# Optimization experiments

Measured on AMD Instinct MI355X. Metric: run time of the kernel, lower is better.

## Reference

```python
import jax, jax.numpy as jnp
import numpy as np

ALPHA = 1.0
BETA = 10.0
OHEM_RATIO = 3
DB_K = 50.0
EPS_P = 1e-7  # clamp probs so log() stays finite (torch BCELoss clamps log at -100)

N, H, W = 16, 640, 640


def setup_inputs() -> dict:
    key = jax.random.key(0)
    k1, k2, k3, k4 = jax.random.split(key, 4)
    return {
        "outputs": jax.random.uniform(k1, (N, 2, H, W), dtype=jnp.float32),
        "labels": jax.random.uniform(k2, (N, 2, H, W), dtype=jnp.float32),
        "training_masks": jax.random.uniform(k3, (N, H, W), dtype=jnp.float32),
        "G_d": jax.random.uniform(k4, (N, H, W), dtype=jnp.float32),
    }


def _ohem_single(score, gt, tm):
    # score, gt, tm: [H, W] for one sample
    pos = (gt > 0.5) & (tm > 0.5)
    neg = (gt <= 0.5) & (tm > 0.5)
    pos_num = pos.sum()
    neg_avail = neg.sum()
    neg_num = jnp.minimum(pos_num * OHEM_RATIO, neg_avail)
    # descending sort of negative-pixel scores; non-neg pixels pushed to -inf
    flat = jnp.where(neg, score, -jnp.inf).ravel()
    sorted_desc = jnp.sort(flat)[::-1]
    idx = jnp.clip(neg_num - 1, 0, flat.shape[0] - 1)
    thr = sorted_desc[idx]
    sel = ((score >= thr) & neg) | pos
    sel = jnp.where(neg_num == 0, pos, sel)          # no negatives selectable -> pos only
    sel = jnp.where(pos_num == 0, tm > 0.5, sel)     # no positives -> whole training mask
    return sel


def _masked_bce(p, t, m):
    # masked-mean BCE == gathering masked elems then BCELoss(mean)
    t = (t > 0.5).astype(p.dtype)
    p = jnp.clip(p, EPS_P, 1.0 - EPS_P)
    loss = -(t * jnp.log(p) + (1.0 - t) * jnp.log1p(-p))
    msum = m.sum()
    return jnp.where(msum > 0, (loss * m).sum() / msum, jnp.zeros((), p.dtype))


def reference(outputs, labels, training_masks, G_d):
    prob_map = outputs[:, 0, :, :]
    thres_map = outputs[:, 1, :, :]
    gt_prob = labels[:, 0, :, :]
    gt_thres = labels[:, 1, :, :]

    sel = jax.vmap(_ohem_single)(prob_map, gt_prob, training_masks)
    sel = sel.astype(prob_map.dtype)  # boolean-derived: no gradient path

    loss_prob = _masked_bce(prob_map, gt_prob, sel)
    bin_map = jax.nn.sigmoid(DB_K * (prob_map - thres_map))  # differentiable binarization
    loss_bin = _masked_bce(bin_map, gt_prob, sel)
    loss_thres = (jnp.abs(thres_map - gt_thres) * G_d).sum() / (G_d.sum() + 1e-6)

    loss_all = loss_prob + ALPHA * loss_bin + BETA * loss_thres
    return (loss_all, loss_prob, loss_bin, loss_thres)
```

## Files before the change

### kernel.cpp

```cpp
#include <hip/hip_runtime.h>
#include <math.h>
#include <stdint.h>

#define NS    16
#define HWSZ  409600
#define NF4   102400
#define NBIN  128
#define SLW   (NBIN + 8)
#define CAP   4096
#define BCAP  512
#define SBPS  100
#define GBPS  100
#define PADI  32

typedef unsigned long long u64;
typedef float f32x4 __attribute__((ext_vector_type(4)));

__device__ __forceinline__ unsigned fkey(float f) {
    unsigned u = __float_as_uint(f);
    if (u == 0x80000000u) u = 0u;
    return (u & 0x80000000u) ? ~u : (u | 0x80000000u);
}

__device__ __forceinline__ void bce_pair(float pv, float tv, bool tc, float& o1, float& o2) {
    float pc = fminf(fmaxf(pv, 1e-7f), 1.0f - 1e-7f);
    float a = tc ? pc : 1.0f - pc;
    o1 = -__logf(a);
    float x = 50.0f * (pv - tv);
    float y = tc ? -x : x;
    float t2 = __expf(-fabsf(y));
    float sp = __logf(1.0f + t2);
    sp = (y > 0.0f) ? y + sp : sp;
    o2 = fminf(sp, 16.118095651f);
}

__device__ __forceinline__ int pbin(float p) {
    int b = (int)(p * (float)NBIN);
    return min(max(b, 0), NBIN - 1);
}

__device__ __forceinline__ bool wave_find(const int* __restrict__ h, int nbins, int k,
                                          int* bin_out, int* rank_out) {
    const int lane = threadIdx.x & 63;
    const int CH = nbins >> 6;
    const int topStart = nbins - 1 - lane * CH;
    int s = 0;
    for (int b = 0; b < CH; ++b) s += h[topStart - b];
    int incl = s;
    for (int off = 1; off < 64; off <<= 1) {
        int v = __shfl_up(incl, off, 64);
        if (lane >= off) incl += v;
    }
    int before = incl - s;
    if (before < k && k <= incl) {
        int c = before;
        for (int b = 0; b < CH; ++b) {
            int hb = h[topStart - b];
            c += hb;
            if (c >= k) { *bin_out = topStart - b; *rank_out = k - (c - hb); return true; }
        }
    }
    return false;
}

#define GLOAD(dst, addr) \
    asm volatile("global_load_dwordx4 %0, %1, off" : "=v"(dst) : "v"(addr))
#define LOADSET(Sp, St, Sg, Sq, Sm, Sd, idx) do { \
    GLOAD(Sp, P + (idx));  GLOAD(St, Th + (idx)); GLOAD(Sg, G + (idx)); \
    GLOAD(Sq, Gt + (idx)); GLOAD(Sm, T + (idx)); GLOAD(Sd, D + (idx)); } while (0)
#define WAITSET(Sp, St, Sg, Sq, Sm, Sd, N) \
    asm volatile("s_waitcnt vmcnt(" #N ")" \
                 : "+v"(Sp), "+v"(St), "+v"(Sg), "+v"(Sq), "+v"(Sm), "+v"(Sd))

__global__ void k_scan1(const float* __restrict__ outputs, const float* __restrict__ labels,
                        const float* __restrict__ tmask, const float* __restrict__ gd,
                        float* __restrict__ part) {
    __shared__ int lc[NBIN];
    __shared__ float rf[4][6];
    __shared__ int ri[4][2];
    const int t = threadIdx.x, n = blockIdx.y, lane = t & 63, wid = t >> 6;
    if (t < NBIN) lc[t] = 0;
    __syncthreads();
    const f32x4* P  = (const f32x4*)(outputs + (size_t)n * 2 * HWSZ);
    const f32x4* Th = P + NF4;
    const f32x4* G  = (const f32x4*)(labels + (size_t)n * 2 * HWSZ);
    const f32x4* Gt = G + NF4;
    const f32x4* T  = (const f32x4*)(tmask + (size_t)n * HWSZ);
    const f32x4* D  = (const f32x4*)(gd + (size_t)n * HWSZ);
    const int i0 = blockIdx.x * 1024 + t;
    float s3 = 0.f, s4 = 0.f, p1 = 0.f, p2 = 0.f, n1 = 0.f, n2 = 0.f;
    int cp = 0, cn = 0;
    auto proc = [&](const f32x4& p, const f32x4& th, const f32x4& g, const f32x4& q,
                    const f32x4& m, const f32x4& d) {
#pragma unroll
        for (int e = 0; e < 4; ++e) {
            float pv = p[e], tv = th[e], gv = g[e], qv = q[e], mv = m[e], dv = d[e];
            s3 += fabsf(tv - qv) * dv;
            s4 += dv;
            bool msk = mv > 0.5f, tc = gv > 0.5f;
            if (msk) {
                float o1, o2; bce_pair(pv, tv, tc, o1, o2);
                if (tc) { p1 += o1; p2 += o2; cp++; }
                else    { n1 += o1; n2 += o2; cn++; atomicAdd(&lc[pbin(pv)], 1); }
            }
        }
    };
    f32x4 ap, at, ag, aq, am, ad, bp, bt, bg, bq, bm, bd, cq, ct, cg, cqq, cm, cd;
    LOADSET(ap, at, ag, aq, am, ad, i0);
    LOADSET(bp, bt, bg, bq, bm, bd, i0 + 256);
    LOADSET(cq, ct, cg, cqq, cm, cd, i0 + 512);
    WAITSET(ap, at, ag, aq, am, ad, 12);
    proc(ap, at, ag, aq, am, ad);
    LOADSET(ap, at, ag, aq, am, ad, i0 + 768);
    WAITSET(bp, bt, bg, bq, bm, bd, 12);
    proc(bp, bt, bg, bq, bm, bd);
    WAITSET(cq, ct, cg, cqq, cm, cd, 6);
    proc(cq, ct, cg, cqq, cm, cd);
    WAITSET(ap, at, ag, aq, am, ad, 0);
    proc(ap, at, ag, aq, am, ad);
    for (int off = 32; off; off >>= 1) {
        p1 += __shfl_down(p1, off, 64);
        p2 += __shfl_down(p2, off, 64);
        n1 += __shfl_down(n1, off, 64);
        n2 += __shfl_down(n2, off, 64);
        s3 += __shfl_down(s3, off, 64);
        s4 += __shfl_down(s4, off, 64);
        cp += __shfl_down(cp, off, 64);
        cn += __shfl_down(cn, off, 64);
    }
    if (!lane) {
        rf[wid][0] = p1; rf[wid][1] = p2; rf[wid][2] = n1;
        rf[wid][3] = n2; rf[wid][4] = s3; rf[wid][5] = s4;
        ri[wid][0] = cp; ri[wid][1] = cn;
    }
    __syncthreads();
    float* slice = part + (size_t)(n * SBPS + blockIdx.x) * SLW;
    int* slice_i = (int*)slice;
    if (t < NBIN) slice_i[t] = lc[t];
    if (!t) {
        slice_i[NBIN + 0] = ri[0][0] + ri[1][0] + ri[2][0] + ri[3][0];
        slice_i[NBIN + 1] = ri[0][1] + ri[1][1] + ri[2][1] + ri[3][1];
#pragma unroll
        for (int i = 0; i < 6; ++i)
            slice[NBIN + 2 + i] = rf[0][i] + rf[1][i] + rf[2][i] + rf[3][i];
    }
}

__global__ void k_sel1(const float* __restrict__ part,
                       int* __restrict__ mode, int* __restrict__ b1o, int* __restrict__ k1o,
                       int* __restrict__ poss,
                       double* __restrict__ psum, double* __restrict__ abD, int* __restrict__ abc,
                       double* __restrict__ s3s, double* __restrict__ s4s,
                       int* __restrict__ cand_cnt, unsigned* __restrict__ done) {
    __shared__ int lc[NBIN];
    __shared__ double sdr[4][6];
    __shared__ int sir[4][2];
    __shared__ int ric[4];
    __shared__ int sb1, sk1, s_md, s_k;
    const int n = blockIdx.x, t = threadIdx.x, lane = t & 63, wid = t >> 6;
    if (t < PADI) cand_cnt[n * PADI + t] = 0;
    if (!n && !t) *done = 0u;
    const float* base = part + (size_t)n * SBPS * SLW;
    double v[6] = {0, 0, 0, 0, 0, 0};
    int cp = 0, cn = 0;
    if (t < SBPS) {
        const float* sl = base + (size_t)t * SLW;
        const int* sli = (const int*)sl;
        cp = sli[NBIN + 0]; cn = sli[NBIN + 1];
#pragma unroll
        for (int i = 0; i < 6; ++i) v[i] = (double)sl[NBIN + 2 + i];
    }
    for (int off = 32; off; off >>= 1) {
#pragma unroll
        for (int i = 0; i < 6; ++i) v[i] += __shfl_down(v[i], off, 64);
        cp += __shfl_down(cp, off, 64);
        cn += __shfl_down(cn, off, 64);
    }
    if (!lane) {
#pragma unroll
        for (int i = 0; i < 6; ++i) sdr[wid][i] = v[i];
        sir[wid][0] = cp; sir[wid][1] = cn;
    }
    __syncthreads();
    if (!t) {
        int pos = sir[0][0] + sir[1][0] + sir[2][0] + sir[3][0];
        int neg = sir[0][1] + sir[1][1] + sir[2][1] + sir[3][1];
        double c[6];
#pragma unroll
        for (int i = 0; i < 6; ++i) c[i] = sdr[0][i] + sdr[1][i] + sdr[2][i] + sdr[3][i];
        int k = pos * 3; if (k > neg) k = neg;
        int md = (pos == 0) ? 2 : ((k == 0) ? 1 : ((k == neg) ? 3 : 0));
        mode[n] = md;
        poss[n] = pos;
        psum[n * 2 + 0] = c[0];
        psum[n * 2 + 1] = c[1];
        s3s[n] = c[4];
        s4s[n] = c[5];
        if (md == 1)      { abD[n * 16] = 0.0;  abD[n * 16 + 1] = 0.0;  abc[n] = 0; }
        else if (md != 0) { abD[n * 16] = c[2]; abD[n * 16 + 1] = c[3]; abc[n] = neg; }
        else              { abD[n * 16] = 0.0;  abD[n * 16 + 1] = 0.0; }
        s_md = md; s_k = k;
    }
    __syncthreads();
    if (s_md != 0) return;
    if (t < NBIN) lc[t] = 0;
    __syncthreads();
    {
        const int bin = t & (NBIN - 1);
        const int j0 = (t < NBIN) ? 0 : SBPS / 2;
        const int j1 = (t < NBIN) ? SBPS / 2 : SBPS;
        int c = 0;
        for (int j = j0; j < j1; ++j) c += ((const int*)(base + (size_t)j * SLW))[bin];
        atomicAdd(&lc[bin], c);
    }
    __syncthreads();
    if (t < 64) { int b, r; if (wave_find(lc, NBIN, s_k, &b, &r)) { sb1 = b; sk1 = r; } }
    __syncthreads();
    const int B = sb1;
    if (!t) { b1o[n] = sb1; k1o[n] = sk1; }
    int ac = (t < NBIN && t > B) ? lc[t] : 0;
    for (int off = 32; off; off >>= 1) ac += __shfl_down(ac, off, 64);
    if (!lane) ric[wid] = ac;
    __syncthreads();
    if (!t) abc[n] = ric[0] + ric[1] + ric[2] + ric[3];
}

__global__ void k_gather(const float* __restrict__ outputs, const float* __restrict__ labels,
                         const float* __restrict__ tmask,
                         const int* __restrict__ mode, const int* __restrict__ b1a,
                         int* __restrict__ cand_cnt, unsigned* __restrict__ ck,
                         float* __restrict__ cv1, float* __restrict__ cv2,
                         double* __restrict__ abD) {
    const int n = blockIdx.y;
    if (mode[n] != 0) return;
    const int b1n = b1a[n];
    __shared__ int lcnt, lbase;
    __shared__ unsigned lsk[BCAP];
    __shared__ float lv1[BCAP], lv2[BCAP];
    __shared__ double rdd[4][2];
    const int t = threadIdx.x, lane = t & 63, wid = t >> 6;
    if (!t) lcnt = 0;
    __syncthreads();
    const float* bp = outputs + (size_t)n * 2 * HWSZ;
    const float4* P  = (const float4*)bp;
    const float4* Th = P + NF4;
    const float4* G  = (const float4*)(labels + (size_t)n * 2 * HWSZ);
    const float4* T  = (const float4*)(tmask + (size_t)n * HWSZ);
    const int stride = GBPS * 256;
    float a1 = 0.f, a2 = 0.f;
    for (int i4 = blockIdx.x * 256 + t; i4 < NF4; i4 += stride) {
        float4 p = P[i4], th = Th[i4], g = G[i4], m = T[i4];
        const float* pp = (const float*)&p;  const float* tt = (const float*)&th;
        const float* gg = (const float*)&g;  const float* mm = (const float*)&m;
#pragma unroll
        for (int e = 0; e < 4; ++e) {
            bool neg = (gg[e] <= 0.5f) && (mm[e] > 0.5f);
            int bin = pbin(pp[e]);
            if (neg && bin >= b1n) {
                float o1, o2; bce_pair(pp[e], tt[e], false, o1, o2);
                if (bin > b1n) { a1 += o1; a2 += o2; }
                else {
                    int idx = atomicAdd(&lcnt, 1);
                    if (idx < BCAP) { lsk[idx] = fkey(pp[e]); lv1[idx] = o1; lv2[idx] = o2; }
                    else {
                        int gi = atomicAdd(&cand_cnt[n * PADI], 1);
                        if (gi < CAP) { ck[n * CAP + gi] = fkey(pp[e]); cv1[n * CAP + gi] = o1; cv2[n * CAP + gi] = o2; }
                    }
                }
            }
        }
    }
    double v0 = a1, v1 = a2;
    for (int off = 32; off; off >>= 1) {
        v0 += __shfl_down(v0, off, 64);
        v1 += __shfl_down(v1, off, 64);
    }
    if (!lane) { rdd[wid][0] = v0; rdd[wid][1] = v1; }
    __syncthreads();
    if (!t) {
        double sA = rdd[0][0] + rdd[1][0] + rdd[2][0] + rdd[3][0];
        double sB = rdd[0][1] + rdd[1][1] + rdd[2][1] + rdd[3][1];
        if (sA != 0.0) atomicAdd(&abD[n * 16], sA);
        if (sB != 0.0) atomicAdd(&abD[n * 16 + 1], sB);
    }
    __syncthreads();
    const int cnt = min(lcnt, BCAP);
    if (!t && cnt) lbase = atomicAdd(&cand_cnt[n * PADI], cnt);
    __syncthreads();
    if (cnt) {
        const int bb = lbase;
        for (int i = t; i < cnt; i += 256) {
            int gi = bb + i;
            if (gi < CAP) { ck[n * CAP + gi] = lsk[i]; cv1[n * CAP + gi] = lv1[i]; cv2[n * CAP + gi] = lv2[i]; }
        }
    }
}

__global__ void k_final(const float* __restrict__ outputs, const float* __restrict__ labels,
                        const float* __restrict__ tmask,
                        const int* __restrict__ mode, const int* __restrict__ b1a,
                        const int* __restrict__ k1a, const int* __restrict__ poss,
                        const int* __restrict__ cand_cnt, const unsigned* __restrict__ ck,
                        const float* __restrict__ cv1, const float* __restrict__ cv2,
                        const double* __restrict__ psum, const double* __restrict__ abD,
                        const int* __restrict__ abc, double* __restrict__ res,
                        const double* __restrict__ s3s, const double* __restrict__ s4s,
                        unsigned* __restrict__ done, float* __restrict__ out) {
    __shared__ unsigned sk[CAP];
    __shared__ float sv1[CAP], sv2[CAP];
    __shared__ int h[2048];
    __shared__ int sbh, srh, sbm, srm, sbl;
    __shared__ double rd[4][2];
    __shared__ int ri[4];
    const int n = blockIdx.x, t = threadIdx.x;
    const int md = mode[n];
    double f1r = 0.0, f2r = 0.0; int fcr = 0;
    if (md == 0) {
        const int k1 = k1a[n];
        const int cc = cand_cnt[n * PADI];
        float f1 = 0.f, f2 = 0.f; int fc = 0;
        if (cc <= CAP) {
            for (int i = t; i < cc; i += 256) {
                sk[i] = ck[n * CAP + i]; sv1[i] = cv1[n * CAP + i]; sv2[i] = cv2[n * CAP + i];
            }
            for (int i = t; i < 2048; i += 256) h[i] = 0;
            __syncthreads();
            for (int i = t; i < cc; i += 256) atomicAdd(&h[sk[i] >> 21], 1);
            __syncthreads();
            if (t < 64) { int b, r; if (wave_find(h, 2048, k1, &b, &r)) { sbh = b; srh = r; } }
            __syncthreads();
            const unsigned bh = (unsigned)sbh; const int r2 = srh;
            for (int i = t; i < 2048; i += 256) h[i] = 0;
            __syncthreads();
            for (int i = t; i < cc; i += 256)
                if ((sk[i] >> 21) == bh) atomicAdd(&h[(sk[i] >> 10) & 0x7FFu], 1);
            __syncthreads();
            if (t < 64) { int b, r; if (wave_find(h, 2048, r2, &b, &r)) { sbm = b; srm = r; } }
            __syncthreads();
            const unsigned bm = (unsigned)sbm; const int r3 = srm;
            for (int i = t; i < 1024; i += 256) h[i] = 0;
            __syncthreads();
            for (int i = t; i < cc; i += 256)
                if ((sk[i] >> 10) == ((bh << 11) | bm)) atomicAdd(&h[sk[i] & 0x3FFu], 1);
            __syncthreads();
            if (t < 64) { int b, r; if (wave_find(h, 1024, r3, &b, &r)) sbl = b; }
            __syncthreads();
            const unsigned thr_key = (bh << 21) | (bm << 10) | (unsigned)sbl;
            for (int i = t; i < cc; i += 256)
                if (sk[i] >= thr_key) { f1 += sv1[i]; f2 += sv2[i]; fc++; }
        } else {
            const int b1n = b1a[n];
            const float* Pp = outputs + (size_t)n * 2 * HWSZ;
            const float* Thp = Pp + HWSZ;
            const float* Gp = labels + (size_t)n * 2 * HWSZ;
            const float* Tp = tmask + (size_t)n * HWSZ;
            for (int i = t; i < 2048; i += 256) h[i] = 0;
            __syncthreads();
            for (int i = t; i < HWSZ; i += 256) {
                float pv = Pp[i];
                if (Gp[i] <= 0.5f && Tp[i] > 0.5f && pbin(pv) == b1n)
                    atomicAdd(&h[fkey(pv) >> 21], 1);
            }
            __syncthreads();
            if (t < 64) { int b, r; if (wave_find(h, 2048, k1, &b, &r)) { sbh = b; srh = r; } }
            __syncthreads();
            const unsigned bh = (unsigned)sbh; const int r2 = srh;
            for (int i = t; i < 2048; i += 256) h[i] = 0;
            __syncthreads();
            for (int i = t; i < HWSZ; i += 256) {
                float pv = Pp[i]; unsigned key = fkey(pv);
                if (Gp[i] <= 0.5f && Tp[i] > 0.5f && pbin(pv) == b1n && (key >> 21) == bh)
                    atomicAdd(&h[(key >> 10) & 0x7FFu], 1);
            }
            __syncthreads();
            if (t < 64) { int b, r; if (wave_find(h, 2048, r2, &b, &r)) { sbm = b; srm = r; } }
            __syncthreads();
            const unsigned bm = (unsigned)sbm; const int r3 = srm;
            for (int i = t; i < 1024; i += 256) h[i] = 0;
            __syncthreads();
            for (int i = t; i < HWSZ; i += 256) {
                float pv = Pp[i]; unsigned key = fkey(pv);
                if (Gp[i] <= 0.5f && Tp[i] > 0.5f && pbin(pv) == b1n && (key >> 10) == ((bh << 11) | bm))
                    atomicAdd(&h[key & 0x3FFu], 1);
            }
            __syncthreads();
            if (t < 64) { int b, r; if (wave_find(h, 1024, r3, &b, &r)) sbl = b; }
            __syncthreads();
            const unsigned thr_key = (bh << 21) | (bm << 10) | (unsigned)sbl;
            for (int i = t; i < HWSZ; i += 256) {
                float pv = Pp[i];
                if (Gp[i] <= 0.5f && Tp[i] > 0.5f && pbin(pv) == b1n && fkey(pv) >= thr_key) {
                    float b1v, b2v; bce_pair(pv, Thp[i], false, b1v, b2v);
                    f1 += b1v; f2 += b2v; fc++;
                }
            }
        }
        double v0 = f1, v1 = f2;
        for (int off = 32; off; off >>= 1) {
            v0 += __shfl_down(v0, off, 64);
            v1 += __shfl_down(v1, off, 64);
            fc += __shfl_down(fc, off, 64);
        }
        const int lane = t & 63, wid = t >> 6;
        if (!lane) { rd[wid][0] = v0; rd[wid][1] = v1; ri[wid] = fc; }
        __syncthreads();
        if (!t) {
            f1r = rd[0][0] + rd[1][0] + rd[2][0] + rd[3][0];
            f2r = rd[0][1] + rd[1][1] + rd[2][1] + rd[3][1];
            fcr = ri[0] + ri[1] + ri[2] + ri[3];
        }
    }
    if (!t) {
        res[n * 3 + 0] = psum[n * 2 + 0] + abD[n * 16] + f1r;
        res[n * 3 + 1] = psum[n * 2 + 1] + abD[n * 16 + 1] + f2r;
        res[n * 3 + 2] = (double)poss[n] + (double)abc[n] + (double)fcr;
        __threadfence();
        unsigned v = atomicAdd(done, 1u);
        if (v == NS - 1) {
            __threadfence();
            double A = 0.0, Bb = 0.0, C = 0.0, S3 = 0.0, S4 = 0.0;
            for (int m = 0; m < NS; ++m) {
                A += res[m * 3 + 0]; Bb += res[m * 3 + 1]; C += res[m * 3 + 2];
                S3 += s3s[m]; S4 += s4s[m];
            }
            double lp = (C > 0.0) ? A / C : 0.0;
            double lb = (C > 0.0) ? Bb / C : 0.0;
            double lt = S3 / (S4 + 1e-6);
            out[0] = (float)(lp + lb + 10.0 * lt);
            out[1] = (float)lp;
            out[2] = (float)lb;
            out[3] = (float)lt;
        }
    }
}

extern "C" void kernel_launch(void* const* d_in, const int* in_sizes, int n_in,
                              void* d_out, int out_size, void* d_ws, size_t ws_size,
                              hipStream_t stream) {
    const float* outputs = (const float*)d_in[0];
    const float* labels  = (const float*)d_in[1];
    const float* tmask   = (const float*)d_in[2];
    const float* gd      = (const float*)d_in[3];
    float* out = (float*)d_out;

    char* ws = (char*)d_ws;
    double* s3s   = (double*)ws;
    double* s4s   = s3s + NS;
    double* psum  = s4s + NS;
    double* abD   = psum + NS * 2;
    double* res   = abD + NS * 16;
    int* abc      = (int*)(res + NS * 3);
    int* mode     = abc + NS;
    int* b1       = mode + NS;
    int* k1       = b1 + NS;
    int* poss     = k1 + NS;
    unsigned* done = (unsigned*)(poss + NS);
    int* cand_cnt = (int*)(done + 8);
    float* part   = (float*)(cand_cnt + NS * PADI);
    unsigned* ck  = (unsigned*)(part + (size_t)NS * SBPS * SLW);
    float* cv1    = (float*)(ck + NS * CAP);
    float* cv2    = cv1 + NS * CAP;
    (void)cv2; (void)ws_size; (void)in_sizes; (void)n_in; (void)out_size;

    k_scan1<<<dim3(SBPS, NS), 256, 0, stream>>>(outputs, labels, tmask, gd, part);
    k_sel1<<<NS, 256, 0, stream>>>(part, mode, b1, k1, poss, psum, abD, abc, s3s, s4s,
                                   cand_cnt, done);
    k_gather<<<dim3(GBPS, NS), 256, 0, stream>>>(outputs, labels, tmask, mode, b1,
                                                 cand_cnt, ck, cv1, cv2, abD);
    k_final<<<NS, 256, 0, stream>>>(outputs, labels, tmask, mode, b1, k1, poss, cand_cnt,
                                    ck, cv1, cv2, psum, abD, abc, res, s3s, s4s, done, out);
}
```

Measured before the change: 39.03 us.

## Fuse gather and final kernels via last-block counter; enlarge scan1 per-block work

Merges the candidate-gather and final-selection kernels into one launch. A per-sample atomic completion counter picks the last gather block, which then runs the radix-select and final reduction, reading candidates straight from global memory instead of staging them in shared memory. This removes one kernel launch and the gap between launches, but the final work now runs serially in a single block per sample after its gather finishes. Scan1 also cuts its blocks per sample from 100 to 80, with each block handling five load sets instead of four, so there are fewer partial slices to reduce at the cost of lower parallelism.

```diff
diff --git a/kernel.cpp b/kernel.cpp
--- a/kernel.cpp
+++ b/kernel.cpp
@@ -9,7 +9,7 @@
 #define SLW   (NBIN + 8)
 #define CAP   4096
 #define BCAP  512
-#define SBPS  100
+#define SBPS  80
 #define GBPS  100
 #define PADI  32
 
@@ -87,7 +87,7 @@
     const f32x4* Gt = G + NF4;
     const f32x4* T  = (const f32x4*)(tmask + (size_t)n * HWSZ);
     const f32x4* D  = (const f32x4*)(gd + (size_t)n * HWSZ);
-    const int i0 = blockIdx.x * 1024 + t;
+    const int i0 = blockIdx.x * 1280 + t;
     float s3 = 0.f, s4 = 0.f, p1 = 0.f, p2 = 0.f, n1 = 0.f, n2 = 0.f;
     int cp = 0, cn = 0;
     auto proc = [&](const f32x4& p, const f32x4& th, const f32x4& g, const f32x4& q,
@@ -114,10 +114,13 @@
     LOADSET(ap, at, ag, aq, am, ad, i0 + 768);
     WAITSET(bp, bt, bg, bq, bm, bd, 12);
     proc(bp, bt, bg, bq, bm, bd);
-    WAITSET(cq, ct, cg, cqq, cm, cd, 6);
+    LOADSET(bp, bt, bg, bq, bm, bd, i0 + 1024);
+    WAITSET(cq, ct, cg, cqq, cm, cd, 12);
     proc(cq, ct, cg, cqq, cm, cd);
-    WAITSET(ap, at, ag, aq, am, ad, 0);
+    WAITSET(ap, at, ag, aq, am, ad, 6);
     proc(ap, at, ag, aq, am, ad);
+    WAITSET(bp, bt, bg, bq, bm, bd, 0);
+    proc(bp, bt, bg, bq, bm, bd);
     for (int off = 32; off; off >>= 1) {
         p1 += __shfl_down(p1, off, 64);
         p2 += __shfl_down(p2, off, 64);
@@ -151,7 +154,8 @@
                        int* __restrict__ poss,
                        double* __restrict__ psum, double* __restrict__ abD, int* __restrict__ abc,
                        double* __restrict__ s3s, double* __restrict__ s4s,
-                       int* __restrict__ cand_cnt, unsigned* __restrict__ done) {
+                       int* __restrict__ cand_cnt, unsigned* __restrict__ gdone,
+                       unsigned* __restrict__ fdone) {
     __shared__ int lc[NBIN];
     __shared__ double sdr[4][6];
     __shared__ int sir[4][2];
@@ -159,7 +163,7 @@
     __shared__ int sb1, sk1, s_md, s_k;
     const int n = blockIdx.x, t = threadIdx.x, lane = t & 63, wid = t >> 6;
     if (t < PADI) cand_cnt[n * PADI + t] = 0;
-    if (!n && !t) *done = 0u;
+    if (!t) { gdone[n] = 0u; if (!n) *fdone = 0u; }
     const float* base = part + (size_t)n * SBPS * SLW;
     double v[6] = {0, 0, 0, 0, 0, 0};
     int cp = 0, cn = 0;
@@ -225,107 +229,103 @@
     if (!t) abc[n] = ric[0] + ric[1] + ric[2] + ric[3];
 }
 
-__global__ void k_gather(const float* __restrict__ outputs, const float* __restrict__ labels,
-                         const float* __restrict__ tmask,
-                         const int* __restrict__ mode, const int* __restrict__ b1a,
-                         int* __restrict__ cand_cnt, unsigned* __restrict__ ck,
-                         float* __restrict__ cv1, float* __restrict__ cv2,
-                         double* __restrict__ abD) {
-    const int n = blockIdx.y;
-    if (mode[n] != 0) return;
-    const int b1n = b1a[n];
-    __shared__ int lcnt, lbase;
+__global__ void k_gf(const float* __restrict__ outputs, const float* __restrict__ labels,
+                     const float* __restrict__ tmask,
+                     const int* __restrict__ mode, const int* __restrict__ b1a,
+                     const int* __restrict__ k1a, const int* __restrict__ poss,
+                     int* __restrict__ cand_cnt, unsigned* __restrict__ ck,
+                     float* __restrict__ cv1, float* __restrict__ cv2,
+                     double* __restrict__ abD,
+                     const double* __restrict__ psum, const int* __restrict__ abc,
+                     double* __restrict__ res,
+                     const double* __restrict__ s3s, const double* __restrict__ s4s,
+                     unsigned* __restrict__ gdone, unsigned* __restrict__ fdone,
+                     float* __restrict__ out) {
+    __shared__ int lcnt, lbase, s_last;
     __shared__ unsigned lsk[BCAP];
     __shared__ float lv1[BCAP], lv2[BCAP];
     __shared__ double rdd[4][2];
-    const int t = threadIdx.x, lane = t & 63, wid = t >> 6;
-    if (!t) lcnt = 0;
-    __syncthreads();
-    const float* bp = outputs + (size_t)n * 2 * HWSZ;
-    const float4* P  = (const float4*)bp;
-    const float4* Th = P + NF4;
-    const float4* G  = (const float4*)(labels + (size_t)n * 2 * HWSZ);
-    const float4* T  = (const float4*)(tmask + (size_t)n * HWSZ);
-    const int stride = GBPS * 256;
-    float a1 = 0.f, a2 = 0.f;
-    for (int i4 = blockIdx.x * 256 + t; i4 < NF4; i4 += stride) {
-        float4 p = P[i4], th = Th[i4], g = G[i4], m = T[i4];
-        const float* pp = (const float*)&p;  const float* tt = (const float*)&th;
-        const float* gg = (const float*)&g;  const float* mm = (const float*)&m;
-#pragma unroll
-        for (int e = 0; e < 4; ++e) {
-            bool neg = (gg[e] <= 0.5f) && (mm[e] > 0.5f);
-            int bin = pbin(pp[e]);
-            if (neg && bin >= b1n) {
-                float o1, o2; bce_pair(pp[e], tt[e], false, o1, o2);
-                if (bin > b1n) { a1 += o1; a2 += o2; }
-                else {
-                    int idx = atomicAdd(&lcnt, 1);
-                    if (idx < BCAP) { lsk[idx] = fkey(pp[e]); lv1[idx] = o1; lv2[idx] = o2; }
-                    else {
-                        int gi = atomicAdd(&cand_cnt[n * PADI], 1);
-                        if (gi < CAP) { ck[n * CAP + gi] = fkey(pp[e]); cv1[n * CAP + gi] = o1; cv2[n * CAP + gi] = o2; }
-                    }
-                }
-            }
-        }
-    }
-    double v0 = a1, v1 = a2;
-    for (int off = 32; off; off >>= 1) {
-        v0 += __shfl_down(v0, off, 64);
-        v1 += __shfl_down(v1, off, 64);
-    }
-    if (!lane) { rdd[wid][0] = v0; rdd[wid][1] = v1; }
-    __syncthreads();
-    if (!t) {
-        double sA = rdd[0][0] + rdd[1][0] + rdd[2][0] + rdd[3][0];
-        double sB = rdd[0][1] + rdd[1][1] + rdd[2][1] + rdd[3][1];
-        if (sA != 0.0) atomicAdd(&abD[n * 16], sA);
-        if (sB != 0.0) atomicAdd(&abD[n * 16 + 1], sB);
-    }
-    __syncthreads();
-    const int cnt = min(lcnt, BCAP);
-    if (!t && cnt) lbase = atomicAdd(&cand_cnt[n * PADI], cnt);
-    __syncthreads();
-    if (cnt) {
-        const int bb = lbase;
-        for (int i = t; i < cnt; i += 256) {
-            int gi = bb + i;
-            if (gi < CAP) { ck[n * CAP + gi] = lsk[i]; cv1[n * CAP + gi] = lv1[i]; cv2[n * CAP + gi] = lv2[i]; }
-        }
-    }
-}
-
-__global__ void k_final(const float* __restrict__ outputs, const float* __restrict__ labels,
-                        const float* __restrict__ tmask,
-                        const int* __restrict__ mode, const int* __restrict__ b1a,
-                        const int* __restrict__ k1a, const int* __restrict__ poss,
-                        const int* __restrict__ cand_cnt, const unsigned* __restrict__ ck,
-                        const float* __restrict__ cv1, const float* __restrict__ cv2,
-                        const double* __restrict__ psum, const double* __restrict__ abD,
-                        const int* __restrict__ abc, double* __restrict__ res,
-                        const double* __restrict__ s3s, const double* __restrict__ s4s,
-                        unsigned* __restrict__ done, float* __restrict__ out) {
-    __shared__ unsigned sk[CAP];
-    __shared__ float sv1[CAP], sv2[CAP];
     __shared__ int h[2048];
     __shared__ int sbh, srh, sbm, srm, sbl;
     __shared__ double rd[4][2];
     __shared__ int ri[4];
-    const int n = blockIdx.x, t = threadIdx.x;
+    const int n = blockIdx.y, t = threadIdx.x, lane = t & 63, wid = t >> 6;
     const int md = mode[n];
+    if (md == 0) {
+        const int b1n = b1a[n];
+        if (!t) lcnt = 0;
+        __syncthreads();
+        const float* bp = outputs + (size_t)n * 2 * HWSZ;
+        const float4* P  = (const float4*)bp;
+        const float4* Th = P + NF4;
+        const float4* G  = (const float4*)(labels + (size_t)n * 2 * HWSZ);
+        const float4* T  = (const float4*)(tmask + (size_t)n * HWSZ);
+        const int stride = GBPS * 256;
+        float a1 = 0.f, a2 = 0.f;
+        for (int i4 = blockIdx.x * 256 + t; i4 < NF4; i4 += stride) {
+            float4 p = P[i4], th = Th[i4], g = G[i4], m = T[i4];
+            const float* pp = (const float*)&p;  const float* tt = (const float*)&th;
+            const float* gg = (const float*)&g;  const float* mm = (const float*)&m;
+#pragma unroll
+            for (int e = 0; e < 4; ++e) {
+                bool neg = (gg[e] <= 0.5f) && (mm[e] > 0.5f);
+                int bin = pbin(pp[e]);
+                if (neg && bin >= b1n) {
+                    float o1, o2; bce_pair(pp[e], tt[e], false, o1, o2);
+                    if (bin > b1n) { a1 += o1; a2 += o2; }
+                    else {
+                        int idx = atomicAdd(&lcnt, 1);
+                        if (idx < BCAP) { lsk[idx] = fkey(pp[e]); lv1[idx] = o1; lv2[idx] = o2; }
+                        else {
+                            int gi = atomicAdd(&cand_cnt[n * PADI], 1);
+                            if (gi < CAP) { ck[n * CAP + gi] = fkey(pp[e]); cv1[n * CAP + gi] = o1; cv2[n * CAP + gi] = o2; }
+                        }
+                    }
+                }
+            }
+        }
+        double v0 = a1, v1 = a2;
+        for (int off = 32; off; off >>= 1) {
+            v0 += __shfl_down(v0, off, 64);
+            v1 += __shfl_down(v1, off, 64);
+        }
+        if (!lane) { rdd[wid][0] = v0; rdd[wid][1] = v1; }
+        __syncthreads();
+        if (!t) {
+            double sA = rdd[0][0] + rdd[1][0] + rdd[2][0] + rdd[3][0];
+            double sB = rdd[0][1] + rdd[1][1] + rdd[2][1] + rdd[3][1];
+            if (sA != 0.0) atomicAdd(&abD[n * 16], sA);
+            if (sB != 0.0) atomicAdd(&abD[n * 16 + 1], sB);
+        }
+        __syncthreads();
+        const int cnt = min(lcnt, BCAP);
+        if (!t && cnt) lbase = atomicAdd(&cand_cnt[n * PADI], cnt);
+        __syncthreads();
+        if (cnt) {
+            const int bb = lbase;
+            for (int i = t; i < cnt; i += 256) {
+                int gi = bb + i;
+                if (gi < CAP) { ck[n * CAP + gi] = lsk[i]; cv1[n * CAP + gi] = lv1[i]; cv2[n * CAP + gi] = lv2[i]; }
+            }
+        }
+    }
+    __syncthreads();
+    if (!t) { __threadfence(); s_last = (atomicAdd(&gdone[n], 1u) == GBPS - 1) ? 1 : 0; }
+    __syncthreads();
+    if (!s_last) return;
+    __threadfence();
     double f1r = 0.0, f2r = 0.0; int fcr = 0;
     if (md == 0) {
         const int k1 = k1a[n];
         const int cc = cand_cnt[n * PADI];
+        const unsigned* ckn = ck + n * CAP;
+        const float* c1n = cv1 + n * CAP;
+        const float* c2n = cv2 + n * CAP;
         float f1 = 0.f, f2 = 0.f; int fc = 0;
         if (cc <= CAP) {
-            for (int i = t; i < cc; i += 256) {
-                sk[i] = ck[n * CAP + i]; sv1[i] = cv1[n * CAP + i]; sv2[i] = cv2[n * CAP + i];
-            }
             for (int i = t; i < 2048; i += 256) h[i] = 0;
             __syncthreads();
-            for (int i = t; i < cc; i += 256) atomicAdd(&h[sk[i] >> 21], 1);
+            for (int i = t; i < cc; i += 256) atomicAdd(&h[ckn[i] >> 21], 1);
             __syncthreads();
             if (t < 64) { int b, r; if (wave_find(h, 2048, k1, &b, &r)) { sbh = b; srh = r; } }
             __syncthreads();
@@ -333,7 +333,7 @@
             for (int i = t; i < 2048; i += 256) h[i] = 0;
             __syncthreads();
             for (int i = t; i < cc; i += 256)
-                if ((sk[i] >> 21) == bh) atomicAdd(&h[(sk[i] >> 10) & 0x7FFu], 1);
+                if ((ckn[i] >> 21) == bh) atomicAdd(&h[(ckn[i] >> 10) & 0x7FFu], 1);
             __syncthreads();
             if (t < 64) { int b, r; if (wave_find(h, 2048, r2, &b, &r)) { sbm = b; srm = r; } }
             __syncthreads();
@@ -341,13 +341,13 @@
             for (int i = t; i < 1024; i += 256) h[i] = 0;
             __syncthreads();
             for (int i = t; i < cc; i += 256)
-                if ((sk[i] >> 10) == ((bh << 11) | bm)) atomicAdd(&h[sk[i] & 0x3FFu], 1);
+                if ((ckn[i] >> 10) == ((bh << 11) | bm)) atomicAdd(&h[ckn[i] & 0x3FFu], 1);
             __syncthreads();
             if (t < 64) { int b, r; if (wave_find(h, 1024, r3, &b, &r)) sbl = b; }
             __syncthreads();
             const unsigned thr_key = (bh << 21) | (bm << 10) | (unsigned)sbl;
             for (int i = t; i < cc; i += 256)
-                if (sk[i] >= thr_key) { f1 += sv1[i]; f2 += sv2[i]; fc++; }
+                if (ckn[i] >= thr_key) { f1 += c1n[i]; f2 += c2n[i]; fc++; }
         } else {
             const int b1n = b1a[n];
             const float* Pp = outputs + (size_t)n * 2 * HWSZ;
@@ -401,7 +401,6 @@
             v1 += __shfl_down(v1, off, 64);
             fc += __shfl_down(fc, off, 64);
         }
-        const int lane = t & 63, wid = t >> 6;
         if (!lane) { rd[wid][0] = v0; rd[wid][1] = v1; ri[wid] = fc; }
         __syncthreads();
         if (!t) {
@@ -415,7 +414,7 @@
         res[n * 3 + 1] = psum[n * 2 + 1] + abD[n * 16 + 1] + f2r;
         res[n * 3 + 2] = (double)poss[n] + (double)abc[n] + (double)fcr;
         __threadfence();
-        unsigned v = atomicAdd(done, 1u);
+        unsigned v = atomicAdd(fdone, 1u);
         if (v == NS - 1) {
             __threadfence();
             double A = 0.0, Bb = 0.0, C = 0.0, S3 = 0.0, S4 = 0.0;
@@ -454,8 +453,9 @@
     int* b1       = mode + NS;
     int* k1       = b1 + NS;
     int* poss     = k1 + NS;
-    unsigned* done = (unsigned*)(poss + NS);
-    int* cand_cnt = (int*)(done + 8);
+    unsigned* gdone = (unsigned*)(poss + NS);
+    unsigned* fdone = gdone + NS;
+    int* cand_cnt = (int*)(fdone + 8);
     float* part   = (float*)(cand_cnt + NS * PADI);
     unsigned* ck  = (unsigned*)(part + (size_t)NS * SBPS * SLW);
     float* cv1    = (float*)(ck + NS * CAP);
@@ -464,9 +464,8 @@
 
     k_scan1<<<dim3(SBPS, NS), 256, 0, stream>>>(outputs, labels, tmask, gd, part);
     k_sel1<<<NS, 256, 0, stream>>>(part, mode, b1, k1, poss, psum, abD, abc, s3s, s4s,
-                                   cand_cnt, done);
-    k_gather<<<dim3(GBPS, NS), 256, 0, stream>>>(outputs, labels, tmask, mode, b1,
-                                                 cand_cnt, ck, cv1, cv2, abD);
-    k_final<<<NS, 256, 0, stream>>>(outputs, labels, tmask, mode, b1, k1, poss, cand_cnt,
-                                    ck, cv1, cv2, psum, abD, abc, res, s3s, s4s, done, out);
-}
+                                   cand_cnt, gdone, fdone);
+    k_gf<<<dim3(GBPS, NS), 256, 0, stream>>>(outputs, labels, tmask, mode, b1, k1, poss,
+                                             cand_cnt, ck, cv1, cv2, abD, psum, abc, res,
+                                             s3s, s4s, gdone, fdone, out);
+}
```

After: 69.02 us. 76.8% more time.
